# Optimization experiments

Hardware: AMD Instinct MI355X
Metric: run time of the kernel (lower is better)

The kernel has to match this reference:

```python
import jax, jax.numpy as jnp
import numpy as np

B, V, E = 64, 16384, 524288          # batch cells, genes (graph nodes), edges
CL1_F, CL1_K = 32, 6                  # cheby conv out-features, polynomial order
POOL = 8
FC1Fin = CL1_F * (V // POOL)          # 65536
FC1_F, FC2_F = 512, 512
NN_FC1, NN_FC2 = 1024, 512
OUT = 10


def _linear_params(k, fout, fin):
    k1, k2 = jax.random.split(k)
    s = 1.0 / np.sqrt(fin)
    w = jax.random.uniform(k1, (fout, fin), minval=-s, maxval=s, dtype=jnp.float32)
    b = jax.random.uniform(k2, (fout,), minval=-s, maxval=s, dtype=jnp.float32)
    return w, b


def setup_inputs() -> dict:
    key = jax.random.key(0)
    ks = jax.random.split(key, 12)
    cl1_w, cl1_b = _linear_params(ks[0], CL1_F, CL1_K)
    fc1_w, fc1_b = _linear_params(ks[1], FC1_F, FC1Fin)
    fc2_w, fc2_b = _linear_params(ks[2], FC2_F, FC1_F)
    fc3_w, fc3_b = _linear_params(ks[3], V, FC2_F)
    nn1_w, nn1_b = _linear_params(ks[4], NN_FC1, V)
    nn2_w, nn2_b = _linear_params(ks[5], NN_FC2, NN_FC1)
    sum2_w, sum2_b = _linear_params(ks[6], OUT, FC1_F + NN_FC2)
    x_in = jax.random.normal(ks[7], (B, V), dtype=jnp.float32)
    L_rows = jax.random.randint(ks[8], (E,), 0, V, dtype=jnp.int32)
    L_cols = jax.random.randint(ks[9], (E,), 0, V, dtype=jnp.int32)
    # values of the rescaled Laplacian 2L/lmax - I (preprocessing done on host)
    L_vals = jax.random.normal(ks[10], (E,), dtype=jnp.float32) * 0.01
    return dict(x_in=x_in, L_vals=L_vals,
                cl1_w=cl1_w, cl1_b=cl1_b, fc1_w=fc1_w, fc1_b=fc1_b,
                fc2_w=fc2_w, fc2_b=fc2_b, fc3_w=fc3_w, fc3_b=fc3_b,
                nn1_w=nn1_w, nn1_b=nn1_b, nn2_w=nn2_w, nn2_b=nn2_b,
                sum2_w=sum2_w, sum2_b=sum2_b,
                L_rows=L_rows, L_cols=L_cols)


def _spmm(vals, rows, cols, x):
    # sparse [V,V] @ dense [V,B] via gather + segment_sum
    return jax.ops.segment_sum(vals[:, None] * x[cols], rows, num_segments=V)


def reference(x_in, L_vals, cl1_w, cl1_b, fc1_w, fc1_b, fc2_w, fc2_b,
              fc3_w, fc3_b, nn1_w, nn1_b, nn2_w, nn2_b, sum2_w, sum2_b,
              L_rows, L_cols):
    # --- graph_conv_cheby (Fin = 1) ---
    x0 = x_in.T                      # [V, B]  (== view of [V, Fin*B])
    xs = [x0]
    x1 = _spmm(L_vals, L_rows, L_cols, x0)
    xs.append(x1)
    for _ in range(2, CL1_K):
        x2 = 2.0 * _spmm(L_vals, L_rows, L_cols, x1) - x0
        xs.append(x2)
        x0, x1 = x1, x2
    xc = jnp.stack(xs, 0)            # [K, V, B]
    xc = xc.transpose(2, 1, 0)       # [B, V, K]
    x = xc @ cl1_w.T + cl1_b         # [B, V, CL1_F]
    x = jax.nn.relu(x)
    # --- graph_max_pool(p=8) over node dim ---
    x = x.reshape(B, V // POOL, POOL, CL1_F).max(axis=2)   # [B, V/8, CL1_F]
    x = x.reshape(B, FC1Fin)
    # --- GAE hidden + decode branch ---
    x_hidden = jax.nn.relu(x @ fc1_w.T + fc1_b)            # [B, FC1_F]
    xd = jax.nn.relu(x_hidden @ fc2_w.T + fc2_b)           # FC2_F != 0 path
    # Dropout(d) with d=0 -> identity (deterministic reference)
    x_decode = xd @ fc3_w.T + fc3_b                        # [B, V]
    # --- plain NN branch on raw input ---
    xn = jax.nn.relu(x_in @ nn1_w.T + nn1_b)
    xn = jax.nn.relu(xn @ nn2_w.T + nn2_b)                 # [B, NN_FC2]
    # --- fuse + classify ---
    xcat = jnp.concatenate([x_hidden, xn], axis=1)
    logp = jax.nn.log_softmax(xcat @ sum2_w.T + sum2_b, axis=1)  # [B, OUT]
    return x_decode, x_hidden, logp
```

## Files before the change

### kernel.cpp

```cpp
#include <hip/hip_runtime.h>

#define B_    64
#define V_    16384
#define E_    524288
#define KCH   6
#define FCH   32
#define FIN1  65536
#define FC1F  512
#define FC2F  512
#define NN1F  1024
#define NN2F  512
#define OUTC  10
#define KT2   64

#define OFF_XS      0u
#define OFF_SCOL    12582912u
#define OFF_SVAL    13631488u
#define OFF_RSTART  14680064u
#define OFF_CNT     14746112u
#define OFF_CF      14811648u
#define OFF_SLICE   15073792u
#define OFF_XD      15073792u
#define OFF_XN1     15204864u
#define OFF_XN2     15467008u

typedef __attribute__((ext_vector_type(4))) float v4f;
typedef __attribute__((ext_vector_type(2))) float v2f;
typedef __attribute__((ext_vector_type(4))) unsigned short u16x4;

__device__ __forceinline__ float b2f(unsigned short h) {
    union { unsigned int u; float f; } v; v.u = ((unsigned int)h) << 16; return v.f;
}
__device__ __forceinline__ unsigned short f2b(float f) {
    union { float f; unsigned int u; } v; v.f = f;
    unsigned int u = v.u;
    u += 0x7fffu + ((u >> 16) & 1u);
    return (unsigned short)(u >> 16);
}

__global__ void prep_k(const float* __restrict__ xin, unsigned short* __restrict__ x0) {
    __shared__ unsigned short tl[64][65];
    int t = threadIdx.x;
    int v0 = blockIdx.x * 64;
    #pragma unroll
    for (int i = 0; i < 16; i++) {
        int idx = t + i * 256;
        int b = idx >> 6, v = idx & 63;
        tl[v][b] = f2b(xin[(size_t)b * V_ + v0 + v]);
    }
    __syncthreads();
    #pragma unroll
    for (int i = 0; i < 16; i++) {
        int idx = t + i * 256;
        int v = idx >> 6, b = idx & 63;
        x0[(size_t)(v0 + v) * B_ + b] = tl[v][b];
    }
}

__global__ void count_k(const int* __restrict__ rows, int* __restrict__ cnt) {
    int e = blockIdx.x * 256 + threadIdx.x;
    if (e < E_) atomicAdd(&cnt[rows[e] & (V_ - 1)], 1);
}

__global__ void scan_k(int* __restrict__ cnt_cursor, int* __restrict__ row_start) {
    __shared__ int sums[256];
    int t = threadIdx.x;
    int loc[64];
    int s = 0;
    #pragma unroll
    for (int i = 0; i < 64; i++) { loc[i] = cnt_cursor[t * 64 + i]; s += loc[i]; }
    sums[t] = s;
    __syncthreads();
    for (int off = 1; off < 256; off <<= 1) {
        int v = (t >= off) ? sums[t - off] : 0;
        __syncthreads();
        sums[t] += v;
        __syncthreads();
    }
    int base = (t == 0) ? 0 : sums[t - 1];
    #pragma unroll
    for (int i = 0; i < 64; i++) {
        row_start[t * 64 + i] = base;
        cnt_cursor[t * 64 + i] = base;
        base += loc[i];
    }
    if (t == 255) row_start[V_] = base;
}

__global__ void scatter_k(const int* __restrict__ rows, const int* __restrict__ cols,
                          const float* __restrict__ vals,
                          int* __restrict__ cursor, unsigned short* __restrict__ scol,
                          unsigned short* __restrict__ sval) {
    int e = blockIdx.x * 256 + threadIdx.x;
    if (e < E_) {
        int r = rows[e] & (V_ - 1);
        int p = atomicAdd(&cursor[r], 1);
        scol[p] = (unsigned short)(cols[e] & (V_ - 1));
        sval[p] = f2b(vals[e]);
    }
}

__global__ void spmm_k(const int* __restrict__ row_start, const unsigned short* __restrict__ scol,
                       const unsigned short* __restrict__ sval,
                       const unsigned short* __restrict__ x,
                       const unsigned short* __restrict__ xprev, unsigned short* __restrict__ y,
                       int mode) {
    int row  = blockIdx.x * 4 + (threadIdx.x >> 6);
    int lane = threadIdx.x & 63;
    int s = row_start[row], e = row_start[row + 1];
    float a0 = 0.f, a1 = 0.f, a2 = 0.f, a3 = 0.f;
    int i = s;
    for (; i + 4 <= e; i += 4) {
        int c0 = scol[i], c1 = scol[i + 1], c2 = scol[i + 2], c3 = scol[i + 3];
        float v0 = b2f(sval[i]), v1 = b2f(sval[i + 1]);
        float v2 = b2f(sval[i + 2]), v3 = b2f(sval[i + 3]);
        a0 += v0 * b2f(x[(size_t)c0 * B_ + lane]);
        a1 += v1 * b2f(x[(size_t)c1 * B_ + lane]);
        a2 += v2 * b2f(x[(size_t)c2 * B_ + lane]);
        a3 += v3 * b2f(x[(size_t)c3 * B_ + lane]);
    }
    for (; i < e; i++)
        a0 += b2f(sval[i]) * b2f(x[(size_t)scol[i] * B_ + lane]);
    float acc = (a0 + a1) + (a2 + a3);
    size_t o = (size_t)row * B_ + lane;
    float r = mode ? (2.f * acc - b2f(xprev[o])) : acc;
    y[o] = f2b(r);
}

__global__ void cheby_slice_k(const unsigned short* __restrict__ xs, const float* __restrict__ w,
                              const float* __restrict__ bias, unsigned short* __restrict__ slice,
                              int g) {
    __shared__ float tile[KCH * 512];
    __shared__ float wf[FCH * KCH];
    __shared__ float bf[FCH];
    int t = threadIdx.x;
    int vpl = blockIdx.x;
    int vp = g * 256 + vpl;
    for (int i = t; i < KCH * 512; i += 256) {
        int k = i >> 9, rem = i & 511;
        tile[i] = b2f(xs[(size_t)k * V_ * B_ + (size_t)vp * 512 + rem]);
    }
    if (t < FCH * KCH) wf[t] = w[t];
    if (t < FCH) bf[t] = bias[t];
    __syncthreads();
    int f = t & 31, b0 = t >> 5;
    float wr[KCH];
    #pragma unroll
    for (int k = 0; k < KCH; k++) wr[k] = wf[f * KCH + k];
    float bb = bf[f];
    #pragma unroll
    for (int bi = 0; bi < 8; bi++) {
        int b = b0 * 8 + bi;
        float m = -1e30f;
        #pragma unroll
        for (int j = 0; j < 8; j++) {
            float s = bb;
            #pragma unroll
            for (int k = 0; k < KCH; k++) s += tile[k * 512 + j * 64 + b] * wr[k];
            m = fmaxf(m, s);
        }
        slice[(size_t)b * 8192 + vpl * FCH + f] = f2b(fmaxf(m, 0.f));
    }
}

__global__ void gemm3_k(const void* __restrict__ Av, int a32, int lda, int ka0,
                        const float* __restrict__ W, int ldw, int kw0,
                        int klen, int N, const float* __restrict__ bias,
                        int relu, int direct, int accum,
                        float* __restrict__ Cp, float* __restrict__ Co) {
    __shared__ float As[KT2][68];
    __shared__ float Ws[KT2][36];
    const unsigned short* Au = (const unsigned short*)Av;
    const float* Af = (const float*)Av;
    int t = threadIdx.x;
    int nb = blockIdx.x * 32;
    int ka = ka0 + blockIdx.y * klen;
    int kw = kw0 + blockIdx.y * klen;
    int kq = t & 15;
    int r0 = t >> 4;
    int tm = (t & 31) << 1;
    int tn = (t >> 5) << 2;
    float acc[2][4] = {{0.f, 0.f, 0.f, 0.f}, {0.f, 0.f, 0.f, 0.f}};
    for (int kt = 0; kt < klen; kt += KT2) {
        __syncthreads();
        int kk = kq << 2;
        #pragma unroll
        for (int p = 0; p < 4; p++) {
            int row = r0 + p * 16;
            float a0, a1, a2, a3;
            if (a32) {
                v4f v = *(const v4f*)(Af + (size_t)row * lda + ka + kt + kk);
                a0 = v[0]; a1 = v[1]; a2 = v[2]; a3 = v[3];
            } else {
                u16x4 h = *(const u16x4*)(Au + (size_t)row * lda + ka + kt + kk);
                a0 = b2f(h[0]); a1 = b2f(h[1]); a2 = b2f(h[2]); a3 = b2f(h[3]);
            }
            As[kk + 0][row] = a0; As[kk + 1][row] = a1;
            As[kk + 2][row] = a2; As[kk + 3][row] = a3;
        }
        #pragma unroll
        for (int p = 0; p < 2; p++) {
            int row = r0 + p * 16;
            v4f w = *(const v4f*)(W + (size_t)(nb + row) * ldw + kw + kt + kk);
            Ws[kk + 0][row] = w[0]; Ws[kk + 1][row] = w[1];
            Ws[kk + 2][row] = w[2]; Ws[kk + 3][row] = w[3];
        }
        __syncthreads();
        #pragma unroll 8
        for (int k = 0; k < KT2; k++) {
            v2f a = *(const v2f*)&As[k][tm];
            v4f w = *(const v4f*)&Ws[k][tn];
            #pragma unroll
            for (int i = 0; i < 2; i++)
                #pragma unroll
                for (int j = 0; j < 4; j++)
                    acc[i][j] += a[i] * w[j];
        }
    }
    if (direct) {
        #pragma unroll
        for (int i = 0; i < 2; i++) {
            int m = tm + i;
            v4f v;
            #pragma unroll
            for (int j = 0; j < 4; j++) {
                float x = acc[i][j] + bias[nb + tn + j];
                v[j] = relu ? fmaxf(x, 0.f) : x;
            }
            *(v4f*)(Co + (size_t)m * N + nb + tn) = v;
        }
    } else {
        float* base = Cp + (size_t)blockIdx.y * 64 * N;
        #pragma unroll
        for (int i = 0; i < 2; i++) {
            int m = tm + i;
            float* p = base + (size_t)m * N + nb + tn;
            v4f v;
            if (accum) {
                v4f old = *(const v4f*)p;
                #pragma unroll
                for (int j = 0; j < 4; j++) v[j] = old[j] + acc[i][j];
            } else {
                #pragma unroll
                for (int j = 0; j < 4; j++) v[j] = acc[i][j];
            }
            *(v4f*)p = v;
        }
    }
}

__global__ void finish2_k(const float* __restrict__ Cp, int Y, int len,
                          const float* __restrict__ bias, int nmask, int relu,
                          float* __restrict__ o) {
    int i = blockIdx.x * 256 + threadIdx.x;
    float s = bias[i & nmask];
    for (int y = 0; y < Y; y++) s += Cp[(size_t)y * len + i];
    if (relu) s = fmaxf(s, 0.f);
    o[i] = s;
}

__global__ void sum2_k(const float* __restrict__ xh, const float* __restrict__ xn,
                       const float* __restrict__ w, const float* __restrict__ bias,
                       float* __restrict__ out) {
    int b = blockIdx.x;
    int lane = threadIdx.x;
    float xc[16];
    #pragma unroll
    for (int j = 0; j < 8; j++) xc[j] = xh[b * FC1F + j * 64 + lane];
    #pragma unroll
    for (int j = 0; j < 8; j++) xc[8 + j] = xn[b * NN2F + j * 64 + lane];
    float logits[OUTC];
    #pragma unroll
    for (int o = 0; o < OUTC; o++) {
        float s = 0.f;
        #pragma unroll
        for (int j = 0; j < 16; j++) s += xc[j] * w[o * 1024 + j * 64 + lane];
        #pragma unroll
        for (int off = 32; off; off >>= 1) s += __shfl_xor(s, off);
        logits[o] = s + bias[o];
    }
    float mx = logits[0];
    #pragma unroll
    for (int o = 1; o < OUTC; o++) mx = fmaxf(mx, logits[o]);
    float lse = 0.f;
    #pragma unroll
    for (int o = 0; o < OUTC; o++) lse += expf(logits[o] - mx);
    float lg = logf(lse) + mx;
    if (lane < OUTC) out[b * OUTC + lane] = logits[lane] - lg;
}

extern "C" void kernel_launch(void* const* d_in, const int* in_sizes, int n_in,
                              void* d_out, int out_size, void* d_ws, size_t ws_size,
                              hipStream_t stream) {
    const float* x_in   = (const float*)d_in[0];
    const float* L_vals = (const float*)d_in[1];
    const float* cl1_w  = (const float*)d_in[2];
    const float* cl1_b  = (const float*)d_in[3];
    const float* fc1_w  = (const float*)d_in[4];
    const float* fc1_b  = (const float*)d_in[5];
    const float* fc2_w  = (const float*)d_in[6];
    const float* fc2_b  = (const float*)d_in[7];
    const float* fc3_w  = (const float*)d_in[8];
    const float* fc3_b  = (const float*)d_in[9];
    const float* nn1_w  = (const float*)d_in[10];
    const float* nn1_b  = (const float*)d_in[11];
    const float* nn2_w  = (const float*)d_in[12];
    const float* nn2_b  = (const float*)d_in[13];
    const float* sum2_w = (const float*)d_in[14];
    const float* sum2_b = (const float*)d_in[15];
    const int* L_rows = (const int*)d_in[16];
    const int* L_cols = (const int*)d_in[17];
    float* out = (float*)d_out;
    char* ws = (char*)d_ws;

    unsigned short* xs     = (unsigned short*)(ws + OFF_XS);
    unsigned short* scol   = (unsigned short*)(ws + OFF_SCOL);
    unsigned short* sval   = (unsigned short*)(ws + OFF_SVAL);
    int*            rstart = (int*)(ws + OFF_RSTART);
    int*            cnt    = (int*)(ws + OFF_CNT);
    unsigned short* slice  = (unsigned short*)(ws + OFF_SLICE);
    float*          xd     = (float*)(ws + OFF_XD);
    float*          xn1    = (float*)(ws + OFF_XN1);
    float*          xn2    = (float*)(ws + OFF_XN2);
    float*          cp_a   = (float*)(ws + OFF_SCOL);
    float*          cp_b   = (float*)(ws + OFF_XS);

    float* out_decode = out;
    float* out_hidden = out + (size_t)B_ * V_;
    float* out_logp   = out_hidden + B_ * FC1F;

    prep_k<<<V_ / 64, 256, 0, stream>>>(x_in, xs);

    hipMemsetAsync(cnt, 0, V_ * sizeof(int), stream);
    count_k<<<E_ / 256, 256, 0, stream>>>(L_rows, cnt);
    scan_k<<<1, 256, 0, stream>>>(cnt, rstart);
    scatter_k<<<E_ / 256, 256, 0, stream>>>(L_rows, L_cols, L_vals, cnt, scol, sval);

    size_t VB = (size_t)V_ * B_;
    spmm_k<<<V_ / 4, 256, 0, stream>>>(rstart, scol, sval, xs, nullptr, xs + VB, 0);
    for (int k = 2; k < KCH; k++)
        spmm_k<<<V_ / 4, 256, 0, stream>>>(rstart, scol, sval,
                                           xs + (k - 1) * VB, xs + (k - 2) * VB, xs + k * VB, 1);

    for (int g = 0; g < 8; g++) {
        cheby_slice_k<<<256, 256, 0, stream>>>(xs, cl1_w, cl1_b, slice, g);
        gemm3_k<<<dim3(FC1F / 32, 16), 256, 0, stream>>>(slice, 0, 8192, 0,
                                                         fc1_w, FIN1, g * 8192,
                                                         512, FC1F, nullptr, 0, 0, g ? 1 : 0,
                                                         cp_a, nullptr);
    }
    finish2_k<<<B_ * FC1F / 256, 256, 0, stream>>>(cp_a, 16, B_ * FC1F, fc1_b, FC1F - 1, 1, out_hidden);

    gemm3_k<<<dim3(FC2F / 32, 8), 256, 0, stream>>>(out_hidden, 1, FC1F, 0,
                                                    fc2_w, FC1F, 0,
                                                    64, FC2F, nullptr, 0, 0, 0, cp_a, nullptr);
    finish2_k<<<B_ * FC2F / 256, 256, 0, stream>>>(cp_a, 8, B_ * FC2F, fc2_b, FC2F - 1, 1, xd);

    gemm3_k<<<dim3(V_ / 32, 1), 256, 0, stream>>>(xd, 1, FC2F, 0,
                                                  fc3_w, FC2F, 0,
                                                  FC2F, V_, fc3_b, 0, 1, 0, nullptr, out_decode);

    gemm3_k<<<dim3(NN1F / 32, 32), 256, 0, stream>>>(x_in, 1, V_, 0,
                                                     nn1_w, V_, 0,
                                                     512, NN1F, nullptr, 0, 0, 0, cp_b, nullptr);
    finish2_k<<<B_ * NN1F / 256, 256, 0, stream>>>(cp_b, 32, B_ * NN1F, nn1_b, NN1F - 1, 1, xn1);

    gemm3_k<<<dim3(NN2F / 32, 16), 256, 0, stream>>>(xn1, 1, NN1F, 0,
                                                     nn2_w, NN1F, 0,
                                                     64, NN2F, nullptr, 0, 0, 0, cp_b, nullptr);
    finish2_k<<<B_ * NN2F / 256, 256, 0, stream>>>(cp_b, 16, B_ * NN2F, nn2_b, NN2F - 1, 1, xn2);

    sum2_k<<<B_, 64, 0, stream>>>(out_hidden, xn2, sum2_w, sum2_b, out_logp);
}
```

Before: 870.6 us.

## Fuse prep/count, widen cheby chunks, cut split-K partials and launches

Merges the input transpose and the row-count atomics into one launch. The scatter loop now handles four edges per thread. The cheby+FC1 loop is regrouped from 8 to 4 chunks, with partials stored in the output buffer. The fc2 split-K is replaced by direct bias+relu, the nn2 finish is folded into the logsoftmax kernel, and the GEMM is templated on input precision. These changes target launch overhead and partial-sum traffic, at the cost of different split-K parallelism and reuse of the output buffer as scratch.

```diff
diff --git a/kernel.cpp b/kernel.cpp
--- a/kernel.cpp
+++ b/kernel.cpp
@@ -18,11 +18,9 @@
 #define OFF_SVAL    13631488u
 #define OFF_RSTART  14680064u
 #define OFF_CNT     14746112u
-#define OFF_CF      14811648u
-#define OFF_SLICE   15073792u
 #define OFF_XD      15073792u
 #define OFF_XN1     15204864u
-#define OFF_XN2     15467008u
+#define OFF_CPN2    4194304u
 
 typedef __attribute__((ext_vector_type(4))) float v4f;
 typedef __attribute__((ext_vector_type(2))) float v2f;
@@ -38,37 +36,88 @@
     return (unsigned short)(u >> 16);
 }
 
-__global__ void prep_k(const float* __restrict__ xin, unsigned short* __restrict__ x0) {
-    __shared__ unsigned short tl[64][65];
+template <int A32>
+__device__ __forceinline__ void gemm_block(const void* __restrict__ Av, int lda, int ka,
+                                           const float* __restrict__ W, int ldw, int kw,
+                                           int klen, int nb, char* smem,
+                                           float acc[2][4], int t) {
+    float* As = (float*)smem;
+    float* Ws = (float*)(smem + KT2 * 66 * 4);
+    const unsigned short* Au = (const unsigned short*)Av;
+    const float* Af = (const float*)Av;
+    int kq = t & 15, r0 = t >> 4;
+    int tm = (t & 31) << 1, tn = (t >> 5) << 2;
+    for (int kt = 0; kt < klen; kt += KT2) {
+        __syncthreads();
+        int kk = kq << 2;
+        #pragma unroll
+        for (int p = 0; p < 4; p++) {
+            int row = r0 + p * 16;
+            float a0, a1, a2, a3;
+            if (A32) {
+                v4f v = *(const v4f*)(Af + (size_t)row * lda + ka + kt + kk);
+                a0 = v[0]; a1 = v[1]; a2 = v[2]; a3 = v[3];
+            } else {
+                u16x4 h = *(const u16x4*)(Au + (size_t)row * lda + ka + kt + kk);
+                a0 = b2f(h[0]); a1 = b2f(h[1]); a2 = b2f(h[2]); a3 = b2f(h[3]);
+            }
+            As[(kk + 0) * 66 + row] = a0; As[(kk + 1) * 66 + row] = a1;
+            As[(kk + 2) * 66 + row] = a2; As[(kk + 3) * 66 + row] = a3;
+        }
+        #pragma unroll
+        for (int p = 0; p < 2; p++) {
+            int row = r0 + p * 16;
+            v4f w = *(const v4f*)(W + (size_t)(nb + row) * ldw + kw + kt + kk);
+            Ws[(kk + 0) * 36 + row] = w[0]; Ws[(kk + 1) * 36 + row] = w[1];
+            Ws[(kk + 2) * 36 + row] = w[2]; Ws[(kk + 3) * 36 + row] = w[3];
+        }
+        __syncthreads();
+        #pragma unroll 8
+        for (int k = 0; k < KT2; k++) {
+            v2f a = *(const v2f*)&As[k * 66 + tm];
+            v4f w = *(const v4f*)&Ws[k * 36 + tn];
+            #pragma unroll
+            for (int i = 0; i < 2; i++)
+                #pragma unroll
+                for (int j = 0; j < 4; j++)
+                    acc[i][j] += a[i] * w[j];
+        }
+    }
+}
+
+__global__ void prepcount_k(const float* __restrict__ xin, unsigned short* __restrict__ x0,
+                            const int* __restrict__ rows, int* __restrict__ cnt) {
     int t = threadIdx.x;
-    int v0 = blockIdx.x * 64;
-    #pragma unroll
-    for (int i = 0; i < 16; i++) {
-        int idx = t + i * 256;
-        int b = idx >> 6, v = idx & 63;
-        tl[v][b] = f2b(xin[(size_t)b * V_ + v0 + v]);
-    }
-    __syncthreads();
-    #pragma unroll
-    for (int i = 0; i < 16; i++) {
-        int idx = t + i * 256;
-        int v = idx >> 6, b = idx & 63;
-        x0[(size_t)(v0 + v) * B_ + b] = tl[v][b];
-    }
-}
-
-__global__ void count_k(const int* __restrict__ rows, int* __restrict__ cnt) {
-    int e = blockIdx.x * 256 + threadIdx.x;
-    if (e < E_) atomicAdd(&cnt[rows[e] & (V_ - 1)], 1);
+    int bx = blockIdx.x;
+    if (bx < 256) {
+        __shared__ unsigned short tl[64][65];
+        int v0 = bx * 64;
+        #pragma unroll
+        for (int i = 0; i < 16; i++) {
+            int idx = t + i * 256;
+            int b = idx >> 6, v = idx & 63;
+            tl[v][b] = f2b(xin[(size_t)b * V_ + v0 + v]);
+        }
+        __syncthreads();
+        #pragma unroll
+        for (int i = 0; i < 16; i++) {
+            int idx = t + i * 256;
+            int v = idx >> 6, b = idx & 63;
+            x0[(size_t)(v0 + v) * B_ + b] = tl[v][b];
+        }
+    } else {
+        int idx = (bx - 256) * 256 + t;
+        #pragma unroll
+        for (int h = 0; h < 4; h++)
+            atomicAdd(&cnt[rows[idx + h * 131072] & (V_ - 1)], 1);
+    }
 }
 
 __global__ void scan_k(int* __restrict__ cnt_cursor, int* __restrict__ row_start) {
     __shared__ int sums[256];
     int t = threadIdx.x;
-    int loc[64];
     int s = 0;
-    #pragma unroll
-    for (int i = 0; i < 64; i++) { loc[i] = cnt_cursor[t * 64 + i]; s += loc[i]; }
+    for (int i = 0; i < 64; i++) s += cnt_cursor[t * 64 + i];
     sums[t] = s;
     __syncthreads();
     for (int off = 1; off < 256; off <<= 1) {
@@ -78,11 +127,12 @@
         __syncthreads();
     }
     int base = (t == 0) ? 0 : sums[t - 1];
-    #pragma unroll
     for (int i = 0; i < 64; i++) {
-        row_start[t * 64 + i] = base;
-        cnt_cursor[t * 64 + i] = base;
-        base += loc[i];
+        int idx = t * 64 + i;
+        int c = cnt_cursor[idx];
+        row_start[idx] = base;
+        cnt_cursor[idx] = base;
+        base += c;
     }
     if (t == 255) row_start[V_] = base;
 }
@@ -91,8 +141,10 @@
                           const float* __restrict__ vals,
                           int* __restrict__ cursor, unsigned short* __restrict__ scol,
                           unsigned short* __restrict__ sval) {
-    int e = blockIdx.x * 256 + threadIdx.x;
-    if (e < E_) {
+    int idx = blockIdx.x * 256 + threadIdx.x;
+    #pragma unroll
+    for (int h = 0; h < 4; h++) {
+        int e = idx + h * 131072;
         int r = rows[e] & (V_ - 1);
         int p = atomicAdd(&cursor[r], 1);
         scol[p] = (unsigned short)(cols[e] & (V_ - 1));
@@ -127,15 +179,15 @@
     y[o] = f2b(r);
 }
 
-__global__ void cheby_slice_k(const unsigned short* __restrict__ xs, const float* __restrict__ w,
-                              const float* __restrict__ bias, unsigned short* __restrict__ slice,
-                              int g) {
+__global__ void cheby_q_k(const unsigned short* __restrict__ xs, const float* __restrict__ w,
+                          const float* __restrict__ bias, unsigned short* __restrict__ slice,
+                          int q) {
     __shared__ float tile[KCH * 512];
     __shared__ float wf[FCH * KCH];
     __shared__ float bf[FCH];
     int t = threadIdx.x;
     int vpl = blockIdx.x;
-    int vp = g * 256 + vpl;
+    int vp = q * 512 + vpl;
     for (int i = t; i < KCH * 512; i += 256) {
         int k = i >> 9, rem = i & 511;
         tile[i] = b2f(xs[(size_t)k * V_ * B_ + (size_t)vp * 512 + rem]);
@@ -159,64 +211,24 @@
             for (int k = 0; k < KCH; k++) s += tile[k * 512 + j * 64 + b] * wr[k];
             m = fmaxf(m, s);
         }
-        slice[(size_t)b * 8192 + vpl * FCH + f] = f2b(fmaxf(m, 0.f));
-    }
-}
-
-__global__ void gemm3_k(const void* __restrict__ Av, int a32, int lda, int ka0,
+        slice[(size_t)b * 16384 + vpl * FCH + f] = f2b(fmaxf(m, 0.f));
+    }
+}
+
+__global__ void gemm4_k(const void* __restrict__ Av, int a32, int lda, int ka0,
                         const float* __restrict__ W, int ldw, int kw0,
                         int klen, int N, const float* __restrict__ bias,
                         int relu, int direct, int accum,
                         float* __restrict__ Cp, float* __restrict__ Co) {
-    __shared__ float As[KT2][68];
-    __shared__ float Ws[KT2][36];
-    const unsigned short* Au = (const unsigned short*)Av;
-    const float* Af = (const float*)Av;
+    __shared__ __align__(16) char smem[26112];
     int t = threadIdx.x;
     int nb = blockIdx.x * 32;
     int ka = ka0 + blockIdx.y * klen;
     int kw = kw0 + blockIdx.y * klen;
-    int kq = t & 15;
-    int r0 = t >> 4;
-    int tm = (t & 31) << 1;
-    int tn = (t >> 5) << 2;
+    int tm = (t & 31) << 1, tn = (t >> 5) << 2;
     float acc[2][4] = {{0.f, 0.f, 0.f, 0.f}, {0.f, 0.f, 0.f, 0.f}};
-    for (int kt = 0; kt < klen; kt += KT2) {
-        __syncthreads();
-        int kk = kq << 2;
-        #pragma unroll
-        for (int p = 0; p < 4; p++) {
-            int row = r0 + p * 16;
-            float a0, a1, a2, a3;
-            if (a32) {
-                v4f v = *(const v4f*)(Af + (size_t)row * lda + ka + kt + kk);
-                a0 = v[0]; a1 = v[1]; a2 = v[2]; a3 = v[3];
-            } else {
-                u16x4 h = *(const u16x4*)(Au + (size_t)row * lda + ka + kt + kk);
-                a0 = b2f(h[0]); a1 = b2f(h[1]); a2 = b2f(h[2]); a3 = b2f(h[3]);
-            }
-            As[kk + 0][row] = a0; As[kk + 1][row] = a1;
-            As[kk + 2][row] = a2; As[kk + 3][row] = a3;
-        }
-        #pragma unroll
-        for (int p = 0; p < 2; p++) {
-            int row = r0 + p * 16;
-            v4f w = *(const v4f*)(W + (size_t)(nb + row) * ldw + kw + kt + kk);
-            Ws[kk + 0][row] = w[0]; Ws[kk + 1][row] = w[1];
-            Ws[kk + 2][row] = w[2]; Ws[kk + 3][row] = w[3];
-        }
-        __syncthreads();
-        #pragma unroll 8
-        for (int k = 0; k < KT2; k++) {
-            v2f a = *(const v2f*)&As[k][tm];
-            v4f w = *(const v4f*)&Ws[k][tn];
-            #pragma unroll
-            for (int i = 0; i < 2; i++)
-                #pragma unroll
-                for (int j = 0; j < 4; j++)
-                    acc[i][j] += a[i] * w[j];
-        }
-    }
+    if (a32) gemm_block<1>(Av, lda, ka, W, ldw, kw, klen, nb, smem, acc, t);
+    else     gemm_block<0>(Av, lda, ka, W, ldw, kw, klen, nb, smem, acc, t);
     if (direct) {
         #pragma unroll
         for (int i = 0; i < 2; i++) {
@@ -259,16 +271,23 @@
     o[i] = s;
 }
 
-__global__ void sum2_k(const float* __restrict__ xh, const float* __restrict__ xn,
-                       const float* __restrict__ w, const float* __restrict__ bias,
-                       float* __restrict__ out) {
+__global__ void sum2f_k(const float* __restrict__ xh, const float* __restrict__ cpn,
+                        const float* __restrict__ nn2b,
+                        const float* __restrict__ w, const float* __restrict__ bias,
+                        float* __restrict__ out) {
     int b = blockIdx.x;
     int lane = threadIdx.x;
     float xc[16];
     #pragma unroll
     for (int j = 0; j < 8; j++) xc[j] = xh[b * FC1F + j * 64 + lane];
     #pragma unroll
-    for (int j = 0; j < 8; j++) xc[8 + j] = xn[b * NN2F + j * 64 + lane];
+    for (int j = 0; j < 8; j++) {
+        int n = j * 64 + lane;
+        float s = nn2b[n];
+        #pragma unroll
+        for (int y = 0; y < 4; y++) s += cpn[(size_t)y * (64 * NN2F) + b * NN2F + n];
+        xc[8 + j] = fmaxf(s, 0.f);
+    }
     float logits[OUTC];
     #pragma unroll
     for (int o = 0; o < OUTC; o++) {
@@ -318,57 +337,50 @@
     unsigned short* sval   = (unsigned short*)(ws + OFF_SVAL);
     int*            rstart = (int*)(ws + OFF_RSTART);
     int*            cnt    = (int*)(ws + OFF_CNT);
-    unsigned short* slice  = (unsigned short*)(ws + OFF_SLICE);
     float*          xd     = (float*)(ws + OFF_XD);
     float*          xn1    = (float*)(ws + OFF_XN1);
-    float*          xn2    = (float*)(ws + OFF_XN2);
-    float*          cp_a   = (float*)(ws + OFF_SCOL);
-    float*          cp_b   = (float*)(ws + OFF_XS);
+    unsigned short* sliceq = (unsigned short*)(ws + OFF_SCOL);
+    float*          cp_nn1 = (float*)(ws + OFF_XS);
+    float*          cp_nn2 = (float*)(ws + OFF_CPN2);
 
     float* out_decode = out;
     float* out_hidden = out + (size_t)B_ * V_;
     float* out_logp   = out_hidden + B_ * FC1F;
-
-    prep_k<<<V_ / 64, 256, 0, stream>>>(x_in, xs);
+    float* cp_fc1     = out_decode;
+
+    size_t VB = (size_t)V_ * B_;
 
     hipMemsetAsync(cnt, 0, V_ * sizeof(int), stream);
-    count_k<<<E_ / 256, 256, 0, stream>>>(L_rows, cnt);
+    prepcount_k<<<768, 256, 0, stream>>>(x_in, xs, L_rows, cnt);
     scan_k<<<1, 256, 0, stream>>>(cnt, rstart);
-    scatter_k<<<E_ / 256, 256, 0, stream>>>(L_rows, L_cols, L_vals, cnt, scol, sval);
-
-    size_t VB = (size_t)V_ * B_;
+    scatter_k<<<512, 256, 0, stream>>>(L_rows, L_cols, L_vals, cnt, scol, sval);
     spmm_k<<<V_ / 4, 256, 0, stream>>>(rstart, scol, sval, xs, nullptr, xs + VB, 0);
     for (int k = 2; k < KCH; k++)
         spmm_k<<<V_ / 4, 256, 0, stream>>>(rstart, scol, sval,
                                            xs + (k - 1) * VB, xs + (k - 2) * VB, xs + k * VB, 1);
 
-    for (int g = 0; g < 8; g++) {
-        cheby_slice_k<<<256, 256, 0, stream>>>(xs, cl1_w, cl1_b, slice, g);
-        gemm3_k<<<dim3(FC1F / 32, 16), 256, 0, stream>>>(slice, 0, 8192, 0,
-                                                         fc1_w, FIN1, g * 8192,
-                                                         512, FC1F, nullptr, 0, 0, g ? 1 : 0,
-                                                         cp_a, nullptr);
-    }
-    finish2_k<<<B_ * FC1F / 256, 256, 0, stream>>>(cp_a, 16, B_ * FC1F, fc1_b, FC1F - 1, 1, out_hidden);
-
-    gemm3_k<<<dim3(FC2F / 32, 8), 256, 0, stream>>>(out_hidden, 1, FC1F, 0,
+    for (int q = 0; q < 4; q++) {
+        cheby_q_k<<<512, 256, 0, stream>>>(xs, cl1_w, cl1_b, sliceq, q);
+        gemm4_k<<<dim3(FC1F / 32, 32), 256, 0, stream>>>(sliceq, 0, 16384, 0,
+                                                         fc1_w, FIN1, q * 16384,
+                                                         512, FC1F, nullptr, 0, 0, q ? 1 : 0,
+                                                         cp_fc1, nullptr);
+    }
+    finish2_k<<<B_ * FC1F / 256, 256, 0, stream>>>(cp_fc1, 32, B_ * FC1F, fc1_b, FC1F - 1, 1,
+                                                   out_hidden);
+
+    gemm4_k<<<dim3(FC2F / 32, 1), 256, 0, stream>>>(out_hidden, 1, FC1F, 0,
                                                     fc2_w, FC1F, 0,
-                                                    64, FC2F, nullptr, 0, 0, 0, cp_a, nullptr);
-    finish2_k<<<B_ * FC2F / 256, 256, 0, stream>>>(cp_a, 8, B_ * FC2F, fc2_b, FC2F - 1, 1, xd);
-
-    gemm3_k<<<dim3(V_ / 32, 1), 256, 0, stream>>>(xd, 1, FC2F, 0,
+                                                    FC1F, FC2F, fc2_b, 1, 1, 0, nullptr, xd);
+    gemm4_k<<<dim3(V_ / 32, 1), 256, 0, stream>>>(xd, 1, FC2F, 0,
                                                   fc3_w, FC2F, 0,
                                                   FC2F, V_, fc3_b, 0, 1, 0, nullptr, out_decode);
-
-    gemm3_k<<<dim3(NN1F / 32, 32), 256, 0, stream>>>(x_in, 1, V_, 0,
+    gemm4_k<<<dim3(NN1F / 32, 16), 256, 0, stream>>>(x_in, 1, V_, 0,
                                                      nn1_w, V_, 0,
-                                                     512, NN1F, nullptr, 0, 0, 0, cp_b, nullptr);
-    finish2_k<<<B_ * NN1F / 256, 256, 0, stream>>>(cp_b, 32, B_ * NN1F, nn1_b, NN1F - 1, 1, xn1);
-
-    gemm3_k<<<dim3(NN2F / 32, 16), 256, 0, stream>>>(xn1, 1, NN1F, 0,
-                                                     nn2_w, NN1F, 0,
-                                                     64, NN2F, nullptr, 0, 0, 0, cp_b, nullptr);
-    finish2_k<<<B_ * NN2F / 256, 256, 0, stream>>>(cp_b, 16, B_ * NN2F, nn2_b, NN2F - 1, 1, xn2);
-
-    sum2_k<<<B_, 64, 0, stream>>>(out_hidden, xn2, sum2_w, sum2_b, out_logp);
-}
+                                                     1024, NN1F, nullptr, 0, 0, 0, cp_nn1, nullptr);
+    finish2_k<<<B_ * NN1F / 256, 256, 0, stream>>>(cp_nn1, 16, B_ * NN1F, nn1_b, NN1F - 1, 1, xn1);
+    gemm4_k<<<dim3(NN2F / 32, 4), 256, 0, stream>>>(xn1, 1, NN1F, 0,
+                                                    nn2_w, NN1F, 0,
+                                                    256, NN2F, nullptr, 0, 0, 0, cp_nn2, nullptr);
+    sum2f_k<<<B_, 64, 0, stream>>>(out_hidden, cp_nn2, nn2_b, sum2_w, sum2_b, out_logp);
+}
```

Result: faster. 719.1 us (-17.4%).
